# Performance work log

Hardware: AMD Instinct MI355X
Metric: run time of the kernel (lower is better)

The kernel has to match this reference:

```python
import jax, jax.numpy as jnp
import numpy as np
from math import pi, sqrt, factorial

NUM_SPHERICAL = 7
NUM_RADIAL = 6
CUTOFF = 5.0
ENV_P = 6  # envelope_exponent + 1
E_EDGES = 300000
T_TRIPLETS = 600000

# ---- static numpy precompute: spherical-Bessel zeros + normalizers (DimeNet bessel_basis) ----

def _jn_np(x, n):
    x = np.asarray(x, dtype=np.float64)
    j0 = np.sin(x) / x
    if n == 0:
        return j0
    jm, j = j0, np.sin(x) / x ** 2 - np.cos(x) / x
    for l in range(2, n + 1):
        jm, j = j, (2 * l - 1) / x * j - jm
    return j

def _bessel_zeros(n, k):
    total = k + n - 1
    zeros = np.zeros((n, total))
    zeros[0, :] = np.arange(1, total + 1) * np.pi
    for l in range(1, n):
        for i in range(total - l):
            a, b = zeros[l - 1, i], zeros[l - 1, i + 1]
            fa = _jn_np(a, l)
            for _ in range(80):  # bisection; zeros of j_l interlace zeros of j_{l-1}
                m = 0.5 * (a + b)
                fm = _jn_np(m, l)
                if fa * fm <= 0:
                    b = m
                else:
                    a, fa = m, fm
            zeros[l, i] = 0.5 * (a + b)
    return zeros[:, :k]

_Z = _bessel_zeros(NUM_SPHERICAL, NUM_RADIAL)  # [n, k] zeros z_{l,i}
_NORM = np.stack([1.0 / np.sqrt(0.5 * _jn_np(_Z[l], l + 1) ** 2) for l in range(NUM_SPHERICAL)])
_Z_J = jnp.asarray(_Z, jnp.float32)
_NORM_J = jnp.asarray(_NORM, jnp.float32)

# ---- jnp basis evaluation ----

def _sph_jl(x, l):
    # spherical Bessel j_l via upward recurrence (same closed sin/cos form as sympy lambdify)
    j0 = jnp.sin(x) / x
    if l == 0:
        return j0
    jm, j = j0, jnp.sin(x) / x ** 2 - jnp.cos(x) / x
    for ll in range(2, l + 1):
        jm, j = j, (2 * ll - 1) / x * j - jm
    return j

def _rbf(dist_scaled):
    # [E] -> [E, n, k]; row l = norm_{l,i} * j_l(z_{l,i} * x)
    rows = [_NORM_J[l] * _sph_jl(dist_scaled[:, None] * _Z_J[l], l) for l in range(NUM_SPHERICAL)]
    return jnp.stack(rows, axis=1)

def _assoc_legendre(cost, sint, lmax):
    # Condon-Shortley associated Legendre P_l^m(cos theta), sint = sin(theta) >= 0
    P = {(0, 0): jnp.ones_like(cost)}
    for m in range(1, lmax + 1):
        P[(m, m)] = (1 - 2 * m) * P[(m - 1, m - 1)] * sint
    for m in range(0, lmax):
        P[(m + 1, m)] = (2 * m + 1) * cost * P[(m, m)]
    for m in range(0, lmax + 1):
        for l in range(m + 2, lmax + 1):
            P[(l, m)] = ((2 * l - 1) * cost * P[(l - 1, m)] - (l + m - 1) * P[(l - 2, m)]) / (l - m)
    return P

def _cbf_angle(angle):
    # zero_m_only real spherical harmonics Y_l^0(theta); l=0 column is the constant Y_0^0
    P = _assoc_legendre(jnp.cos(angle), jnp.sin(angle), NUM_SPHERICAL - 1)
    cols = [jnp.full_like(angle, 0.5 / sqrt(pi))]
    for l in range(1, NUM_SPHERICAL):
        cols.append(sqrt((2 * l + 1) / (4.0 * pi)) * P[(l, 0)])
    return jnp.stack(cols, axis=1)  # [T, n]

def _cbf_torsion(angle, phi):
    # full real spherical harmonics, flat order: Y00, then per l: m=-l..l (sin, m=0, cos)
    P = _assoc_legendre(jnp.cos(angle), jnp.sin(angle), NUM_SPHERICAL - 1)
    cols = [jnp.full_like(angle, 0.5 / sqrt(pi))]
    for l in range(1, NUM_SPHERICAL):
        for m in range(-l, l + 1):
            am = abs(m)
            K = sqrt((2 * l + 1) / (4.0 * pi) * factorial(l - am) / factorial(l + am))
            if m < 0:
                cols.append(sqrt(2.0) * K * jnp.sin(am * phi) * P[(l, am)])
            elif m == 0:
                cols.append(K * P[(l, 0)])
            else:
                cols.append(sqrt(2.0) * K * jnp.cos(m * phi) * P[(l, m)])
    return jnp.stack(cols, axis=1)  # [T, n*n]

def setup_inputs() -> dict:
    key = jax.random.key(0)
    k1, k2, k3, k4 = jax.random.split(key, 4)
    dist = jax.random.uniform(k1, (E_EDGES,), jnp.float32, 0.5, CUTOFF)
    angle = jax.random.uniform(k2, (T_TRIPLETS,), jnp.float32, 0.0, pi)
    torsion = jax.random.uniform(k3, (T_TRIPLETS,), jnp.float32, -pi, pi)
    idx_kj = jax.random.randint(k4, (T_TRIPLETS,), 0, E_EDGES, jnp.int32)
    freq = jnp.arange(1, NUM_RADIAL + 1, dtype=jnp.float32) * pi  # DitanceEmbedding param init
    return {"dist": dist, "angle": angle, "torsion": torsion, "freq": freq, "idx_kj": idx_kj}

def reference(dist, angle, torsion, freq, idx_kj):
    n, k = NUM_SPHERICAL, NUM_RADIAL
    p = ENV_P
    a = -(p + 1) * (p + 2) / 2.0   # -28
    b = float(p * (p + 2))         # 48
    c = -p * (p + 1) / 2.0         # -21
    # DitanceEmbedding: envelope(x) * sin(freq * x)
    x = (dist / CUTOFF)[:, None]
    xp0 = x ** (p - 1)
    env = 1.0 / x + a * xp0 + b * xp0 * x + c * xp0 * x * x
    dist_emb = env * jnp.sin(freq * x)                      # [E, k]
    # shared radial basis on scaled dist
    rbf = _rbf(dist / CUTOFF)                               # [E, n, k]
    rbf_g = rbf[idx_kj]                                     # [T, n, k] gather per triplet
    # AngleEmbedding
    cbf_a = _cbf_angle(angle)                               # [T, n]
    angle_emb = (rbf_g * cbf_a[:, :, None]).reshape(-1, n * k)
    # TorsionEmbedding
    cbf_t = _cbf_torsion(angle, torsion).reshape(-1, n, n, 1)
    torsion_emb = (rbf_g[:, None, :, :] * cbf_t).reshape(-1, n * n * k)
    return (dist_emb, angle_emb, torsion_emb)
```

## Files before the change

### kernel.cpp

```cpp
#include <hip/hip_runtime.h>
#include <math.h>

#define NS 7
#define NK 6
#define TW 294
#define TPB 32

typedef float f4 __attribute__((ext_vector_type(4)));

struct ConstTables {
    float zc[42];
    float nc[42];
    float Kc[49];
};

__launch_bounds__(256, 8)
__global__ void fused_kernel(const float* __restrict__ dist,
                             const float* __restrict__ angle,
                             const float* __restrict__ torsion,
                             const float* __restrict__ freq,
                             const int* __restrict__ idx_kj,
                             float* __restrict__ outD,
                             float* __restrict__ outA,
                             float* __restrict__ outT,
                             int E, int T, int NBD,
                             ConstTables ct) {
    __shared__ __align__(16) float smem[2976];
    const int tid = threadIdx.x;

    if (blockIdx.x < NBD) {
        const int e0 = blockIdx.x * 256;
        int e = e0 + tid;
        int ec = e < E ? e : E - 1;
        float x = dist[ec] * 0.2f;
        float inv = 1.0f / x;
        float x2 = x * x;
        float xp0 = x2 * x2 * x;
        float env = inv - 28.0f * xp0 + 48.0f * xp0 * x - 21.0f * xp0 * x2;
        float v[NK];
        #pragma unroll
        for (int i = 0; i < NK; ++i) v[i] = env * __sinf(freq[i] * x);
        if (e0 + 256 <= E) {
            #pragma unroll
            for (int i = 0; i < NK; ++i) smem[tid * 6 + i] = v[i];
            __syncthreads();
            const f4* b4 = (const f4*)smem;
            f4* o4 = (f4*)(outD + (size_t)e0 * 6);
            __builtin_nontemporal_store(b4[tid], o4 + tid);
            if (tid < 128) __builtin_nontemporal_store(b4[256 + tid], o4 + 256 + tid);
        } else if (e < E) {
            #pragma unroll
            for (int i = 0; i < NK; ++i) outD[(size_t)e * 6 + i] = v[i];
        }
        return;
    }

    float* __restrict__ rbf_s = smem;
    float* __restrict__ cbf_s = smem + 1408;
    const int t0 = (blockIdx.x - NBD) * TPB;

    if (tid < TPB) {
        int t = t0 + tid;
        int tc = t < T ? t : T - 1;
        float ang = angle[tc];
        float phi = torsion[tc];

        float st = __sinf(ang), ct_ = __cosf(ang);
        float sp = __sinf(phi), cp = __cosf(phi);
        float sm[NS], cm[NS];
        sm[1] = sp; cm[1] = cp;
        #pragma unroll
        for (int m = 2; m < NS; ++m) {
            sm[m] = sm[m - 1] * cp + cm[m - 1] * sp;
            cm[m] = cm[m - 1] * cp - sm[m - 1] * sp;
        }

        float* cb = cbf_s + tid * 49;
        float pmm = 1.0f;
        #pragma unroll
        for (int m = 0; m < NS; ++m) {
            if (m > 0) pmm = (float)(1 - 2 * m) * pmm * st;
            {
                int f = m * m + m;
                if (m == 0) cb[f] = ct.Kc[f];
                else {
                    cb[f + m] = ct.Kc[f + m] * cm[m] * pmm;
                    cb[f - m] = ct.Kc[f - m] * sm[m] * pmm;
                }
            }
            if (m < NS - 1) {
                float plm1 = pmm;
                float pl = (float)(2 * m + 1) * ct_ * pmm;
                {
                    int l = m + 1, f = l * l + l;
                    if (m == 0) cb[f] = ct.Kc[f] * pl;
                    else {
                        cb[f + m] = ct.Kc[f + m] * cm[m] * pl;
                        cb[f - m] = ct.Kc[f - m] * sm[m] * pl;
                    }
                }
                #pragma unroll
                for (int l = m + 2; l < NS; ++l) {
                    float pn = ((float)(2 * l - 1) * ct_ * pl -
                                (float)(l + m - 1) * plm1) / (float)(l - m);
                    plm1 = pl; pl = pn;
                    int f = l * l + l;
                    if (m == 0) cb[f] = ct.Kc[f] * pl;
                    else {
                        cb[f + m] = ct.Kc[f + m] * cm[m] * pl;
                        cb[f - m] = ct.Kc[f - m] * sm[m] * pl;
                    }
                }
            }
        }
    } else if (tid >= 64 && tid < 64 + 6 * TPB) {
        int w = tid - 64;
        int s = w / 6, p = w - 6 * s;
        int t = t0 + s;
        int tc = t < T ? t : T - 1;
        int idx = idx_kj[tc];
        float x = dist[idx] * 0.2f;
        int jlo = p * 7;
        for (int jj = jlo; jj < jlo + 7; ++jj) {
            int l = jj / 6;
            float arg = ct.zc[jj] * x;
            float s1 = __sinf(arg), c1 = __cosf(arg);
            float inv = 1.0f / arg;
            float j0 = s1 * inv;
            float val = j0;
            if (l >= 1) {
                float jm = j0;
                float jcur = (s1 * inv - c1) * inv;
                for (int ll = 2; ll <= l; ++ll) {
                    float tmp = (float)(2 * ll - 1) * inv * jcur - jm;
                    jm = jcur;
                    jcur = tmp;
                }
                val = jcur;
            }
            rbf_s[s * 44 + jj] = ct.nc[jj] * val;
        }
    }
    __syncthreads();

    int nvalid = T - t0; if (nvalid > TPB) nvalid = TPB;

    if (nvalid == TPB) {
        f4* __restrict__ gT = (f4*)(outT + (size_t)t0 * TW);
        unsigned row = (unsigned)(4 * tid) / 294u;
        unsigned c   = (unsigned)(4 * tid) - row * 294u;
        #pragma unroll
        for (int it = 0; it < 10; ++it) {
            if (it < 9 || tid < 48) {
                unsigned row1 = row, c1 = c + 2;
                if (c1 >= 294u) { c1 -= 294u; row1 += 1; }
                unsigned a0 = c / 42u,  r0 = c - a0 * 42u,  q0 = a0 * 7u + r0 / 6u;
                unsigned a1 = c1 / 42u, r1 = c1 - a1 * 42u, q1 = a1 * 7u + r1 / 6u;
                float qv0 = cbf_s[row * 49 + q0];
                float2 rv0 = *(const float2*)&rbf_s[row * 44 + r0];
                float qv1 = cbf_s[row1 * 49 + q1];
                float2 rv1 = *(const float2*)&rbf_s[row1 * 44 + r1];
                f4 val = { qv0 * rv0.x, qv0 * rv0.y, qv1 * rv1.x, qv1 * rv1.y };
                __builtin_nontemporal_store(val, gT + it * 256 + tid);
            }
            c += 142u; row += 3u;
            if (c >= 294u) { c -= 294u; row += 1u; }
        }
        f4* __restrict__ gA = (f4*)(outA + (size_t)t0 * 42);
        unsigned arow = (unsigned)(4 * tid) / 42u;
        unsigned ac   = (unsigned)(4 * tid) - arow * 42u;
        #pragma unroll
        for (int it = 0; it < 2; ++it) {
            if (it < 1 || tid < 80) {
                unsigned arow1 = arow, ac1 = ac + 2;
                if (ac1 >= 42u) { ac1 -= 42u; arow1 += 1; }
                unsigned l0 = ac / 6u,  qa0 = l0 * l0 + l0;
                unsigned l1 = ac1 / 6u, qa1 = l1 * l1 + l1;
                float qv0 = cbf_s[arow * 49 + qa0];
                float2 rv0 = *(const float2*)&rbf_s[arow * 44 + ac];
                float qv1 = cbf_s[arow1 * 49 + qa1];
                float2 rv1 = *(const float2*)&rbf_s[arow1 * 44 + ac1];
                f4 val = { qv0 * rv0.x, qv0 * rv0.y, qv1 * rv1.x, qv1 * rv1.y };
                __builtin_nontemporal_store(val, gA + it * 256 + tid);
            }
            ac += 16u; arow += 24u;
            if (ac >= 42u) { ac -= 42u; arow += 1u; }
        }
    } else {
        for (int g = tid; g < nvalid * TW; g += 256) {
            int row = g / TW, cc = g - row * TW;
            int a = cc / 42, r = cc - a * 42;
            outT[(size_t)t0 * TW + g] = cbf_s[row * 49 + a * 7 + r / 6] * rbf_s[row * 44 + r];
        }
        for (int g = tid; g < nvalid * 42; g += 256) {
            int row = g / 42, r = g - row * 42;
            int l = r / 6;
            outA[(size_t)t0 * 42 + g] = cbf_s[row * 49 + l * l + l] * rbf_s[row * 44 + r];
        }
    }
}

static double jl_host(double x, int n) {
    double j0 = sin(x) / x;
    if (n == 0) return j0;
    double jm = j0, j = sin(x) / (x * x) - cos(x) / x;
    for (int l = 2; l <= n; ++l) {
        double t = (2.0 * l - 1.0) / x * j - jm;
        jm = j;
        j = t;
    }
    return j;
}

static void compute_tables(ConstTables* ct) {
    const double PI = 3.14159265358979323846;
    double zeros[NS][12];
    const int total = NK + NS - 1;
    for (int i = 0; i < total; ++i) zeros[0][i] = (i + 1) * PI;
    for (int l = 1; l < NS; ++l) {
        for (int i = 0; i < total - l; ++i) {
            double a = zeros[l - 1][i], b = zeros[l - 1][i + 1];
            double fa = jl_host(a, l);
            for (int it = 0; it < 100; ++it) {
                double m = 0.5 * (a + b);
                double fm = jl_host(m, l);
                if (fa * fm <= 0.0) b = m;
                else { a = m; fa = fm; }
            }
            zeros[l][i] = 0.5 * (a + b);
        }
    }
    for (int l = 0; l < NS; ++l) {
        for (int i = 0; i < NK; ++i) {
            double z = zeros[l][i];
            double jn1 = jl_host(z, l + 1);
            ct->zc[l * 6 + i] = (float)z;
            ct->nc[l * 6 + i] = (float)(1.0 / sqrt(0.5 * jn1 * jn1));
        }
    }
    double fact[13];
    fact[0] = 1.0;
    for (int i = 1; i < 13; ++i) fact[i] = fact[i - 1] * (double)i;
    ct->Kc[0] = (float)(0.5 / sqrt(PI));
    for (int l = 1; l < NS; ++l) {
        for (int m = -l; m <= l; ++m) {
            int am = m < 0 ? -m : m;
            double K = sqrt((2.0 * l + 1.0) / (4.0 * PI) * fact[l - am] / fact[l + am]);
            if (m != 0) K *= sqrt(2.0);
            ct->Kc[l * l + m + l] = (float)K;
        }
    }
}

extern "C" void kernel_launch(void* const* d_in, const int* in_sizes, int n_in,
                              void* d_out, int out_size, void* d_ws, size_t ws_size,
                              hipStream_t stream) {
    const float* dist    = (const float*)d_in[0];
    const float* angle   = (const float*)d_in[1];
    const float* torsion = (const float*)d_in[2];
    const float* freq    = (const float*)d_in[3];
    const int*   idx_kj  = (const int*)d_in[4];
    const int E = in_sizes[0];
    const int T = in_sizes[1];
    float* out = (float*)d_out;
    float* outA = out + (size_t)E * NK;
    float* outT = outA + (size_t)T * 42;

    ConstTables ct;
    compute_tables(&ct);

    const int NBT = (T + TPB - 1) / TPB;
    const int NBD = (E + 255) / 256;
    fused_kernel<<<NBD + NBT, 256, 0, stream>>>(dist, angle, torsion, freq, idx_kj,
                                                out, outA, outT, E, T, NBD, ct);
}
```

Baseline: 157.5 us.

## Make triplet work wavefront-local and replace block barrier with LDS waitcnt

Each 64-lane wavefront now owns 8 triplets with its own LDS slice for the rbf and cbf tables. Lanes 0-7 compute the angular basis and lanes 16-63 compute the radial basis. The block-wide __syncthreads is replaced by an lgkmcnt wait plus a scheduling barrier, so waves can move from table building to streaming stores without waiting on each other. In exchange, both table-building branches now diverge inside every wave, and store addressing is recomputed per wave.

```diff
diff --git a/kernel.cpp b/kernel.cpp
--- a/kernel.cpp
+++ b/kernel.cpp
@@ -4,6 +4,7 @@
 #define NS 7
 #define NK 6
 #define TW 294
+#define TPW 8
 #define TPB 32
 
 typedef float f4 __attribute__((ext_vector_type(4)));
@@ -55,12 +56,13 @@
         return;
     }
 
-    float* __restrict__ rbf_s = smem;
-    float* __restrict__ cbf_s = smem + 1408;
-    const int t0 = (blockIdx.x - NBD) * TPB;
-
-    if (tid < TPB) {
-        int t = t0 + tid;
+    const int w = tid >> 6, lane = tid & 63;
+    float* __restrict__ rbf_s = smem + w * 744;
+    float* __restrict__ cbf_s = smem + w * 744 + 352;
+    const int t0w = (blockIdx.x - NBD) * TPB + w * TPW;
+
+    if (lane < TPW) {
+        int t = t0w + lane;
         int tc = t < T ? t : T - 1;
         float ang = angle[tc];
         float phi = torsion[tc];
@@ -75,7 +77,7 @@
             cm[m] = cm[m - 1] * cp - sm[m - 1] * sp;
         }
 
-        float* cb = cbf_s + tid * 49;
+        float* cb = cbf_s + lane * 49;
         float pmm = 1.0f;
         #pragma unroll
         for (int m = 0; m < NS; ++m) {
@@ -113,10 +115,10 @@
                 }
             }
         }
-    } else if (tid >= 64 && tid < 64 + 6 * TPB) {
-        int w = tid - 64;
-        int s = w / 6, p = w - 6 * s;
-        int t = t0 + s;
+    } else if (lane >= 16) {
+        int ww = lane - 16;
+        int s = ww / 6, p = ww - 6 * s;
+        int t = t0w + s;
         int tc = t < T ? t : T - 1;
         int idx = idx_kj[tc];
         float x = dist[idx] * 0.2f;
@@ -141,17 +143,18 @@
             rbf_s[s * 44 + jj] = ct.nc[jj] * val;
         }
     }
-    __syncthreads();
-
-    int nvalid = T - t0; if (nvalid > TPB) nvalid = TPB;
-
-    if (nvalid == TPB) {
-        f4* __restrict__ gT = (f4*)(outT + (size_t)t0 * TW);
-        unsigned row = (unsigned)(4 * tid) / 294u;
-        unsigned c   = (unsigned)(4 * tid) - row * 294u;
+    asm volatile("s_waitcnt lgkmcnt(0)" ::: "memory");
+    __builtin_amdgcn_sched_barrier(0);
+
+    int nvalid = T - t0w; if (nvalid > TPW) nvalid = TPW;
+
+    if (nvalid == TPW) {
+        f4* __restrict__ gT = (f4*)(outT + (size_t)t0w * TW);
+        unsigned row = (unsigned)(4 * lane) / 294u;
+        unsigned c   = (unsigned)(4 * lane) - row * 294u;
         #pragma unroll
         for (int it = 0; it < 10; ++it) {
-            if (it < 9 || tid < 48) {
+            if (it < 9 || lane < 12) {
                 unsigned row1 = row, c1 = c + 2;
                 if (c1 >= 294u) { c1 -= 294u; row1 += 1; }
                 unsigned a0 = c / 42u,  r0 = c - a0 * 42u,  q0 = a0 * 7u + r0 / 6u;
@@ -161,17 +164,18 @@
                 float qv1 = cbf_s[row1 * 49 + q1];
                 float2 rv1 = *(const float2*)&rbf_s[row1 * 44 + r1];
                 f4 val = { qv0 * rv0.x, qv0 * rv0.y, qv1 * rv1.x, qv1 * rv1.y };
-                __builtin_nontemporal_store(val, gT + it * 256 + tid);
-            }
-            c += 142u; row += 3u;
+                __builtin_nontemporal_store(val, gT + it * 64 + lane);
+            }
+            c += 256u; row += 3u;
             if (c >= 294u) { c -= 294u; row += 1u; }
-        }
-        f4* __restrict__ gA = (f4*)(outA + (size_t)t0 * 42);
-        unsigned arow = (unsigned)(4 * tid) / 42u;
-        unsigned ac   = (unsigned)(4 * tid) - arow * 42u;
+            row -= 3u;
+        }
+        f4* __restrict__ gA = (f4*)(outA + (size_t)t0w * 42);
         #pragma unroll
         for (int it = 0; it < 2; ++it) {
-            if (it < 1 || tid < 80) {
+            if (it < 1 || lane < 20) {
+                unsigned flat = (unsigned)(4 * (it * 64 + lane));
+                unsigned arow = flat / 42u, ac = flat - arow * 42u;
                 unsigned arow1 = arow, ac1 = ac + 2;
                 if (ac1 >= 42u) { ac1 -= 42u; arow1 += 1; }
                 unsigned l0 = ac / 6u,  qa0 = l0 * l0 + l0;
@@ -181,21 +185,19 @@
                 float qv1 = cbf_s[arow1 * 49 + qa1];
                 float2 rv1 = *(const float2*)&rbf_s[arow1 * 44 + ac1];
                 f4 val = { qv0 * rv0.x, qv0 * rv0.y, qv1 * rv1.x, qv1 * rv1.y };
-                __builtin_nontemporal_store(val, gA + it * 256 + tid);
-            }
-            ac += 16u; arow += 24u;
-            if (ac >= 42u) { ac -= 42u; arow += 1u; }
+                __builtin_nontemporal_store(val, gA + it * 64 + lane);
+            }
         }
     } else {
-        for (int g = tid; g < nvalid * TW; g += 256) {
+        for (int g = lane; g < nvalid * TW; g += 64) {
             int row = g / TW, cc = g - row * TW;
             int a = cc / 42, r = cc - a * 42;
-            outT[(size_t)t0 * TW + g] = cbf_s[row * 49 + a * 7 + r / 6] * rbf_s[row * 44 + r];
-        }
-        for (int g = tid; g < nvalid * 42; g += 256) {
+            outT[(size_t)t0w * TW + g] = cbf_s[row * 49 + a * 7 + r / 6] * rbf_s[row * 44 + r];
+        }
+        for (int g = lane; g < nvalid * 42; g += 64) {
             int row = g / 42, r = g - row * 42;
             int l = r / 6;
-            outA[(size_t)t0 * 42 + g] = cbf_s[row * 49 + l * l + l] * rbf_s[row * 44 + r];
+            outA[(size_t)t0w * 42 + g] = cbf_s[row * 49 + l * l + l] * rbf_s[row * 44 + r];
         }
     }
 }
```

Measured after the change: 145.2 us. 1.08x faster.
